# Kernel tuning notes

Hardware: AMD Instinct MI355X
Metric: run time of the kernel (lower is better)

## Reference

```python
import jax, jax.numpy as jnp
import numpy as np

N_NODES = 50000
N_EDGES = 800000
IN_F = 128
OUT_F = 128
HEADS = 8
HEAD_DIM = OUT_F // HEADS
EDGE_F = 32


def setup_inputs() -> dict:
    key = jax.random.key(0)
    ks = jax.random.split(key, 14)
    s = lambda fan_in: 1.0 / np.sqrt(fan_in)
    return {
        "node_features": jax.random.normal(ks[0], (N_NODES, IN_F), jnp.float32),
        "edge_index": jax.random.randint(ks[1], (2, N_EDGES), 0, N_NODES, jnp.int64),
        "edge_features": jax.random.normal(ks[2], (N_EDGES, EDGE_F), jnp.float32),
        "Wq": jax.random.uniform(ks[3], (IN_F, OUT_F), jnp.float32, -s(IN_F), s(IN_F)),
        "bq": jnp.zeros((OUT_F,), jnp.float32),
        "Wk": jax.random.uniform(ks[4], (IN_F, OUT_F), jnp.float32, -s(IN_F), s(IN_F)),
        "bk": jnp.zeros((OUT_F,), jnp.float32),
        "Wv": jax.random.uniform(ks[5], (IN_F, OUT_F), jnp.float32, -s(IN_F), s(IN_F)),
        "bv": jnp.zeros((OUT_F,), jnp.float32),
        "We": jax.random.uniform(ks[6], (EDGE_F, HEADS), jnp.float32, -s(EDGE_F), s(EDGE_F)),
        "be": jnp.zeros((HEADS,), jnp.float32),
        "Wo": jax.random.uniform(ks[7], (OUT_F, OUT_F), jnp.float32, -s(OUT_F), s(OUT_F)),
        "bo": jnp.zeros((OUT_F,), jnp.float32),
    }


def reference(node_features, edge_index, edge_features,
              Wq, bq, Wk, bk, Wv, bv, We, be, Wo, bo):
    n_nodes = node_features.shape[0]
    n_edges = edge_index.shape[1]
    sources, targets = edge_index[0], edge_index[1]
    scale = HEAD_DIM ** -0.5

    # dense projections: [n_nodes, heads, head_dim]
    Q = (node_features @ Wq + bq).reshape(n_nodes, HEADS, HEAD_DIM)
    K = (node_features @ Wk + bk).reshape(n_nodes, HEADS, HEAD_DIM)
    V = (node_features @ Wv + bv).reshape(n_nodes, HEADS, HEAD_DIM)

    # gather by edge
    Q_t = Q[targets]           # [n_edges, heads, head_dim]
    K_s = K[sources]
    V_s = V[sources]

    scores = jnp.sum(Q_t * K_s, axis=-1) * scale      # [n_edges, heads]
    scores = scores + (edge_features @ We + be)       # edge bias

    # segment softmax over incoming edges of each target node
    max_s = jax.ops.segment_max(scores, targets, num_segments=n_nodes)
    scores = scores - max_s[targets]
    exp_s = jnp.exp(scores)
    denom = jax.ops.segment_sum(exp_s, targets, num_segments=n_nodes) + 1e-10
    probs = exp_s / denom[targets]                    # [n_edges, heads]

    weighted_V = probs[:, :, None] * V_s              # [n_edges, heads, head_dim]
    aggregated = jax.ops.segment_sum(
        weighted_V.reshape(n_edges, -1), targets, num_segments=n_nodes)
    return aggregated @ Wo + bo
```

## Files before the change

kernel.cpp:

```cpp
#include <hip/hip_runtime.h>

typedef __attribute__((ext_vector_type(8))) short shortx8;
typedef __attribute__((ext_vector_type(4))) float floatx4;
typedef unsigned short u16;
typedef unsigned int u32;

__device__ __forceinline__ float bf2f(unsigned short u) {
    union { unsigned int i; float f; } v; v.i = ((unsigned int)u) << 16; return v.f;
}
__device__ __forceinline__ float bfl(u32 u) {
    union { u32 i; float f; } v; v.i = u << 16; return v.f;
}
__device__ __forceinline__ float bfh(u32 u) {
    union { u32 i; float f; } v; v.i = u & 0xFFFF0000u; return v.f;
}
__device__ __forceinline__ unsigned short f2bf(float f) {
    union { float f; unsigned int i; } v; v.f = f;
    unsigned int x = v.i;
    unsigned int r = x + 0x7FFFu + ((x >> 16) & 1u);
    return (unsigned short)(r >> 16);
}
__device__ __forceinline__ float ldf(const void* p, int i, bool f32) {
    return f32 ? ((const float*)p)[i] : bf2f(((const u16*)p)[i]);
}

__global__ __launch_bounds__(256) void detect_zero_k(
    const u16* __restrict__ nf, const int* __restrict__ ei,
    int* __restrict__ flags, int* __restrict__ deg, int M)
{
    int tid = threadIdx.x;
    if (blockIdx.x != 0) {
        int i = (blockIdx.x - 1) * 256 + tid;
        if (i < M) deg[i] = 0;
        return;
    }
    __shared__ int cnt[2];
    if (tid < 2) cnt[tid] = 0;
    __syncthreads();
    int c0 = 0;
    for (int i = tid; i < 65536; i += 256) {
        u16 v = nf[i];
        if ((v & 0x7F80u) == 0x7F80u) c0++;
    }
    int c1 = 0;
    for (int i = tid; i < 4096; i += 256) {
        if (ei[2 * i + 1] != 0) c1++;
    }
    atomicAdd(&cnt[0], c0);
    atomicAdd(&cnt[1], c1);
    __syncthreads();
    if (tid == 0) {
        flags[0] = (cnt[0] > 8) ? 1 : 0;
        flags[1] = (cnt[1] < 100) ? 1 : 0;
    }
}

__global__ __launch_bounds__(256) void prep_k(
    const void* __restrict__ W0, const void* __restrict__ W1,
    const void* __restrict__ W2, const void* __restrict__ W3,
    const void* __restrict__ b0, const void* __restrict__ b1,
    const void* __restrict__ b2, const void* __restrict__ b3,
    const void* __restrict__ We, const void* __restrict__ be,
    const int* __restrict__ flags,
    u16* __restrict__ WT, float* __restrict__ biasWs,
    float* __restrict__ WeWs, float* __restrict__ beWs)
{
    bool f32 = flags[0] != 0;
    int tid = threadIdx.x;
    if (blockIdx.x < 32) {
        int t = blockIdx.x * 256 + tid;
        int mat  = t >> 11;
        int r    = t & 2047;
        int lane = r & 63;
        int ks   = (r >> 6) & 3;
        int ct   = r >> 8;
        const void* W = (mat == 0) ? W0 : (mat == 1) ? W1 : (mat == 2) ? W2 : W3;
        int k0  = ks * 32 + (lane >> 4) * 8;
        int col = ct * 16 + (lane & 15);
        u16 tmp[8];
#pragma unroll
        for (int j = 0; j < 8; ++j) {
            int off = (k0 + j) * 128 + col;
            tmp[j] = f32 ? f2bf(((const float*)W)[off]) : ((const u16*)W)[off];
        }
        *(shortx8*)(WT + (size_t)t * 8) = *(const shortx8*)tmp;
    } else {
        if (tid < 128) {
            biasWs[0 * 128 + tid] = ldf(b0, tid, f32);
            biasWs[1 * 128 + tid] = ldf(b1, tid, f32);
            biasWs[2 * 128 + tid] = ldf(b2, tid, f32);
            biasWs[3 * 128 + tid] = ldf(b3, tid, f32);
        }
        WeWs[tid] = ldf(We, tid, f32);
        if (tid < 8) beWs[tid] = ldf(be, tid, f32);
    }
}

__global__ __launch_bounds__(256) void hist_ebias_k(
    const int* __restrict__ ei, const void* __restrict__ ef,
    int* __restrict__ deg, int* __restrict__ rank,
    const float* __restrict__ WeWs, const float* __restrict__ beWs,
    float* __restrict__ EBe, int E, const int* __restrict__ flags)
{
    __shared__ float sWe[256];
    __shared__ float sbe[8];
    int tid = threadIdx.x;
    sWe[tid] = WeWs[tid];
    if (tid < 8) sbe[tid] = beWs[tid];
    __syncthreads();

    int e = blockIdx.x * 256 + tid;
    if (e >= E) return;
    bool f32 = flags[0] != 0;
    int tgt = flags[1] ? ei[2 * (E + e)] : ei[E + e];
    rank[e] = atomicAdd(&deg[tgt], 1);

    float v[32];
    if (f32) {
        const floatx4* ep = (const floatx4*)((const float*)ef + (size_t)e * 32);
#pragma unroll
        for (int g = 0; g < 8; ++g) {
            floatx4 t = ep[g];
#pragma unroll
            for (int j = 0; j < 4; ++j) v[g * 4 + j] = t[j];
        }
    } else {
        const shortx8* ep = (const shortx8*)((const u16*)ef + (size_t)e * 32);
#pragma unroll
        for (int g = 0; g < 4; ++g) {
            shortx8 t = ep[g];
#pragma unroll
            for (int j = 0; j < 8; ++j) v[g * 8 + j] = bf2f((unsigned short)t[j]);
        }
    }
    float eb[8];
#pragma unroll
    for (int h = 0; h < 8; ++h) eb[h] = sbe[h];
#pragma unroll
    for (int k = 0; k < 32; ++k)
#pragma unroll
        for (int h = 0; h < 8; ++h) eb[h] += v[k] * sWe[k * 8 + h];

    floatx4* op = (floatx4*)(EBe + (size_t)e * 8);
    op[0] = (floatx4){eb[0], eb[1], eb[2], eb[3]};
    op[1] = (floatx4){eb[4], eb[5], eb[6], eb[7]};
}

__global__ __launch_bounds__(256) void scan1_k(
    const int* __restrict__ deg, int* __restrict__ incl, int* __restrict__ bsum, int M)
{
    __shared__ int s[256];
    int tid = threadIdx.x;
    int i = blockIdx.x * 256 + tid;
    int v = (i < M) ? deg[i] : 0;
    s[tid] = v;
    __syncthreads();
#pragma unroll
    for (int off = 1; off < 256; off <<= 1) {
        int t = (tid >= off) ? s[tid - off] : 0;
        __syncthreads();
        s[tid] += t;
        __syncthreads();
    }
    if (i < M) incl[i] = s[tid];
    if (tid == 255) bsum[blockIdx.x] = s[255];
}

__global__ __launch_bounds__(256) void scan2_k(
    const int* __restrict__ bsum, int* __restrict__ boff, int nb)
{
    __shared__ int s[256];
    int tid = threadIdx.x;
    int v = (tid < nb) ? bsum[tid] : 0;
    s[tid] = v;
    __syncthreads();
#pragma unroll
    for (int off = 1; off < 256; off <<= 1) {
        int t = (tid >= off) ? s[tid - off] : 0;
        __syncthreads();
        s[tid] += t;
        __syncthreads();
    }
    if (tid < nb) boff[tid] = s[tid] - v;
}

__global__ __launch_bounds__(256) void scan3_k(
    const int* __restrict__ incl, const int* __restrict__ boff,
    int* __restrict__ rowptr, int M)
{
    int i = blockIdx.x * 256 + threadIdx.x;
    if (i >= M) return;
    rowptr[i + 1] = incl[i] + boff[i >> 8];
    if (i == 0) rowptr[0] = 0;
}

__global__ __launch_bounds__(256) void qkv_gemm_k(
    const void* __restrict__ A, int M,
    const u16* __restrict__ WT, const float* __restrict__ biasWs,
    u16* __restrict__ Qb, u16* __restrict__ KVb,
    const int* __restrict__ flags)
{
    bool aF32 = flags[0] != 0;
    int lane = threadIdx.x & 63;
    int wave = threadIdx.x >> 6;
    int quad = lane >> 4;
    int l15  = lane & 15;
    int m0   = blockIdx.x * 128 + wave * 32;

    shortx8 afrag[2][4];
#pragma unroll
    for (int mt = 0; mt < 2; ++mt) {
        int row = m0 + mt * 16 + l15;
        row = row < M ? row : M - 1;
#pragma unroll
        for (int ks = 0; ks < 4; ++ks) {
            size_t base = (size_t)row * 128 + ks * 32 + quad * 8;
            if (aF32) {
                const floatx4* ap = (const floatx4*)((const float*)A + base);
                floatx4 f0 = ap[0], f1 = ap[1];
                u16 tmp[8];
#pragma unroll
                for (int j = 0; j < 4; ++j) { tmp[j] = f2bf(f0[j]); tmp[4 + j] = f2bf(f1[j]); }
                afrag[mt][ks] = *(const shortx8*)tmp;
            } else {
                afrag[mt][ks] = *(const shortx8*)((const u16*)A + base);
            }
        }
    }

#pragma unroll
    for (int mat = 0; mat < 3; ++mat) {
        floatx4 acc[2][8];
#pragma unroll
        for (int a = 0; a < 2; ++a)
#pragma unroll
            for (int b = 0; b < 8; ++b)
                acc[a][b] = (floatx4){0.f, 0.f, 0.f, 0.f};
#pragma unroll
        for (int ks = 0; ks < 4; ++ks) {
#pragma unroll
            for (int ct = 0; ct < 8; ++ct) {
                shortx8 bfrag = *(const shortx8*)(WT + (size_t)mat * 16384 +
                                                  ((size_t)(ct * 4 + ks) * 64 + lane) * 8);
                acc[0][ct] = __builtin_amdgcn_mfma_f32_16x16x32_bf16(afrag[0][ks], bfrag, acc[0][ct], 0, 0, 0);
                acc[1][ct] = __builtin_amdgcn_mfma_f32_16x16x32_bf16(afrag[1][ks], bfrag, acc[1][ct], 0, 0, 0);
            }
        }
        u16* base = (mat == 0) ? Qb : (mat == 1) ? KVb : (KVb + 128);
        int stride = (mat == 0) ? 128 : 256;
#pragma unroll
        for (int ct = 0; ct < 8; ++ct) {
            int col = ct * 16 + l15;
            float bs = biasWs[mat * 128 + col];
#pragma unroll
            for (int mt = 0; mt < 2; ++mt) {
#pragma unroll
                for (int r = 0; r < 4; ++r) {
                    int row = m0 + mt * 16 + quad * 4 + r;
                    if (row < M)
                        base[(size_t)row * stride + col] = f2bf(acc[mt][ct][r] + bs);
                }
            }
        }
    }
}

__global__ __launch_bounds__(256) void scatter_k(
    const int* __restrict__ ei, const int* __restrict__ rank,
    const int* __restrict__ rowptr, int2* __restrict__ pr2,
    int E, const int* __restrict__ flags)
{
    int e = blockIdx.x * 256 + threadIdx.x;
    if (e >= E) return;
    bool i64 = flags[1] != 0;
    int src = i64 ? ei[2 * e]       : ei[e];
    int tgt = i64 ? ei[2 * (E + e)] : ei[E + e];
    pr2[rowptr[tgt] + rank[e]] = make_int2(src, e);
}

__global__ __launch_bounds__(256) void node_agg_k(
    const int2* __restrict__ pr2, const int* __restrict__ rowptr,
    const u16* __restrict__ Qb, const u16* __restrict__ KVb,
    const float* __restrict__ EBe, u16* __restrict__ aggN, int M, int E)
{
    int wave = threadIdx.x >> 6;
    int lane = threadIdx.x & 63;
    int n = blockIdx.x * 4 + wave;
    if (n >= M) return;
    int g = lane >> 4;
    int w = lane & 15;
    int h = w >> 1;

    int beg = rowptr[n], end = rowptr[n + 1];
    int pidx = beg + lane;
    if (pidx >= E) pidx = E - 1;
    int2 pv = pr2[pidx];

    uint4 qw = ((const uint4*)(Qb + (size_t)n * 128))[w];
    float q0 = bfl(qw.x), q1 = bfh(qw.x), q2 = bfl(qw.y), q3 = bfh(qw.y);
    float q4 = bfl(qw.z), q5 = bfh(qw.z), q6 = bfl(qw.w), q7 = bfh(qw.w);

    float acc[8];
#pragma unroll
    for (int j = 0; j < 8; ++j) acc[j] = 0.f;
    float dsum = 0.f;

    for (int i = beg; i < end; i += 8) {
        int idxA = i + g;
        int idxB = i + 4 + g;
        bool vA = idxA < end;
        bool vB = idxB < end;
        int cA = vA ? idxA : (end - 1);
        int cB = vB ? idxB : (end - 1);
        int offA = cA - beg;
        int offB = cB - beg;
        int srcA, eidA, srcB, eidB;
        if (offA < 64) { srcA = __shfl(pv.x, offA); eidA = __shfl(pv.y, offA); }
        else           { int2 t = pr2[cA]; srcA = t.x; eidA = t.y; }
        if (offB < 64) { srcB = __shfl(pv.x, offB); eidB = __shfl(pv.y, offB); }
        else           { int2 t = pr2[cB]; srcB = t.x; eidB = t.y; }

        const uint4* kpA = (const uint4*)(KVb + (size_t)srcA * 256);
        const uint4* kpB = (const uint4*)(KVb + (size_t)srcB * 256);
        uint4 kwA = kpA[w];
        uint4 kwB = kpB[w];
        uint4 vwA = kpA[16 + w];
        uint4 vwB = kpB[16 + w];
        float ebA = EBe[(size_t)eidA * 8 + h];
        float ebB = EBe[(size_t)eidB * 8 + h];

        float partA = q0 * bfl(kwA.x) + q1 * bfh(kwA.x)
                    + q2 * bfl(kwA.y) + q3 * bfh(kwA.y)
                    + q4 * bfl(kwA.z) + q5 * bfh(kwA.z)
                    + q6 * bfl(kwA.w) + q7 * bfh(kwA.w);
        float partB = q0 * bfl(kwB.x) + q1 * bfh(kwB.x)
                    + q2 * bfl(kwB.y) + q3 * bfh(kwB.y)
                    + q4 * bfl(kwB.z) + q5 * bfh(kwB.z)
                    + q6 * bfl(kwB.w) + q7 * bfh(kwB.w);
        partA += __shfl_xor(partA, 1);
        partB += __shfl_xor(partB, 1);
        float pA = vA ? __expf(partA * 0.25f + ebA) : 0.f;
        float pB = vB ? __expf(partB * 0.25f + ebB) : 0.f;
        dsum += pA + pB;
        acc[0] += pA * bfl(vwA.x) + pB * bfl(vwB.x);
        acc[1] += pA * bfh(vwA.x) + pB * bfh(vwB.x);
        acc[2] += pA * bfl(vwA.y) + pB * bfl(vwB.y);
        acc[3] += pA * bfh(vwA.y) + pB * bfh(vwB.y);
        acc[4] += pA * bfl(vwA.z) + pB * bfl(vwB.z);
        acc[5] += pA * bfh(vwA.z) + pB * bfh(vwB.z);
        acc[6] += pA * bfl(vwA.w) + pB * bfl(vwB.w);
        acc[7] += pA * bfh(vwA.w) + pB * bfh(vwB.w);
    }

    dsum += __shfl_xor(dsum, 16);
    dsum += __shfl_xor(dsum, 32);
#pragma unroll
    for (int j = 0; j < 8; ++j) {
        acc[j] += __shfl_xor(acc[j], 16);
        acc[j] += __shfl_xor(acc[j], 32);
    }
    if (g == 0) {
        float inv = 1.0f / (dsum + 1e-10f);
        uint4 o;
        o.x = (u32)f2bf(acc[0] * inv) | ((u32)f2bf(acc[1] * inv) << 16);
        o.y = (u32)f2bf(acc[2] * inv) | ((u32)f2bf(acc[3] * inv) << 16);
        o.z = (u32)f2bf(acc[4] * inv) | ((u32)f2bf(acc[5] * inv) << 16);
        o.w = (u32)f2bf(acc[6] * inv) | ((u32)f2bf(acc[7] * inv) << 16);
        ((uint4*)(aggN + (size_t)n * 128))[w] = o;
    }
}

__global__ __launch_bounds__(256) void out_gemm_k(
    const u16* __restrict__ A, int M,
    const u16* __restrict__ WT, const float* __restrict__ bias,
    void* __restrict__ out, const int* __restrict__ flags)
{
    bool oF32 = flags[0] != 0;
    int lane = threadIdx.x & 63;
    int wave = threadIdx.x >> 6;
    int quad = lane >> 4;
    int l15  = lane & 15;
    int m0   = blockIdx.x * 128 + wave * 32;

    floatx4 acc[2][8];
#pragma unroll
    for (int a = 0; a < 2; ++a)
#pragma unroll
        for (int b = 0; b < 8; ++b)
            acc[a][b] = (floatx4){0.f, 0.f, 0.f, 0.f};

#pragma unroll
    for (int ks = 0; ks < 4; ++ks) {
        shortx8 afrag[2];
#pragma unroll
        for (int mt = 0; mt < 2; ++mt) {
            int row = m0 + mt * 16 + l15;
            row = row < M ? row : M - 1;
            afrag[mt] = *(const shortx8*)(A + (size_t)row * 128 + ks * 32 + quad * 8);
        }
#pragma unroll
        for (int ct = 0; ct < 8; ++ct) {
            shortx8 bfrag = *(const shortx8*)(WT + ((size_t)(ct * 4 + ks) * 64 + lane) * 8);
            acc[0][ct] = __builtin_amdgcn_mfma_f32_16x16x32_bf16(afrag[0], bfrag, acc[0][ct], 0, 0, 0);
            acc[1][ct] = __builtin_amdgcn_mfma_f32_16x16x32_bf16(afrag[1], bfrag, acc[1][ct], 0, 0, 0);
        }
    }

#pragma unroll
    for (int ct = 0; ct < 8; ++ct) {
        int col = ct * 16 + l15;
        float bs = bias[col];
#pragma unroll
        for (int mt = 0; mt < 2; ++mt) {
#pragma unroll
            for (int r = 0; r < 4; ++r) {
                int row = m0 + mt * 16 + quad * 4 + r;
                if (row < M) {
                    float v = acc[mt][ct][r] + bs;
                    if (oF32) ((float*)out)[(size_t)row * 128 + col] = v;
                    else      ((u16*)out)[(size_t)row * 128 + col] = f2bf(v);
                }
            }
        }
    }
}

extern "C" void kernel_launch(void* const* d_in, const int* in_sizes, int n_in,
                              void* d_out, int out_size, void* d_ws, size_t ws_size,
                              hipStream_t stream)
{
    const void* nf = d_in[0];
    const int*  ei = (const int*)d_in[1];
    const void* ef = d_in[2];
    const void* Wq = d_in[3];  const void* bq = d_in[4];
    const void* Wk = d_in[5];  const void* bk = d_in[6];
    const void* Wv = d_in[7];  const void* bv = d_in[8];
    const void* We = d_in[9];  const void* be = d_in[10];
    const void* Wo = d_in[11]; const void* bo = d_in[12];

    int M = in_sizes[0] / 128;
    int E = in_sizes[1] / 2;
    int nb = (M + 255) / 256;

    char* ws = (char*)d_ws;
    int*   flags  = (int*)(ws + 0);
    float* biasWs = (float*)(ws + 256);
    float* WeWs   = (float*)(ws + 2304);
    float* beWs   = (float*)(ws + 3328);
    u16*   WT     = (u16*)(ws + 4096);
    size_t O1 = 4096 + 131072;
    size_t qrow  = (size_t)M * 128 * 2;
    size_t kvrow = (size_t)M * 256 * 2;
    u16* Qb  = (u16*)(ws + O1);
    u16* KVb = (u16*)(ws + O1 + qrow);
    size_t O2 = O1 + qrow + kvrow;
    float* EBe = (float*)(ws + O2);
    size_t O3 = O2 + (size_t)E * 8 * 4;
    int2* pr2   = (int2*)(ws + O3);
    int* rank   = (int*)(pr2 + E);
    int* deg    = rank + E;
    int* incl   = deg + M;
    int* rowptr = incl + M;
    int* bsum   = rowptr + M + 1;
    int* boff   = bsum + 256;
    u16* aggN   = Qb;

    detect_zero_k<<<1 + nb, 256, 0, stream>>>((const u16*)nf, ei, flags, deg, M);
    prep_k<<<33, 256, 0, stream>>>(Wq, Wk, Wv, Wo, bq, bk, bv, bo, We, be,
                                   flags, WT, biasWs, WeWs, beWs);

    int eblocks = (E + 255) / 256;
    hist_ebias_k<<<eblocks, 256, 0, stream>>>(ei, ef, deg, rank, WeWs, beWs,
                                              EBe, E, flags);
    scan1_k<<<nb, 256, 0, stream>>>(deg, incl, bsum, M);
    scan2_k<<<1, 256, 0, stream>>>(bsum, boff, nb);
    scan3_k<<<nb, 256, 0, stream>>>(incl, boff, rowptr, M);

    int gblocks = (M + 127) / 128;
    qkv_gemm_k<<<gblocks, 256, 0, stream>>>(nf, M, WT, biasWs, Qb, KVb, flags);

    scatter_k<<<eblocks, 256, 0, stream>>>(ei, rank, rowptr, pr2, E, flags);

    node_agg_k<<<(M + 3) / 4, 256, 0, stream>>>(pr2, rowptr, Qb, KVb, EBe, aggN, M, E);

    out_gemm_k<<<gblocks, 256, 0, stream>>>(aggN, M, WT + 3 * 16384, biasWs + 384, d_out, flags);
}
```

Measured before the change: 443.1 us.

## Fuse prep kernels, scan stages, and QKV GEMM with edge-bias scatter into CSR records

Merges format detection and weight prep into one kernel, folds the scan2/scan3 stages into a single kernel, and runs the QKV GEMM concurrently with a fused edge-bias and scatter pass in one launch. The scatter now uses an atomic cursor per target instead of a precomputed rank, and writes 32-byte records holding the source plus the edge bias packed as bf16, directly in CSR order. The aggregation kernel reads this contiguous bias instead of gathering EBe by edge id. This cuts launches, drops the rank and EBe round trips and removes a random gather, at the cost of bf16 rounding on the bias, a larger record, and a nondeterministic order within each segment.

```diff
diff --git a/kernel.cpp b/kernel.cpp
--- a/kernel.cpp
+++ b/kernel.cpp
@@ -20,55 +20,52 @@
     unsigned int r = x + 0x7FFFu + ((x >> 16) & 1u);
     return (unsigned short)(r >> 16);
 }
+__device__ __forceinline__ u32 pack2bf(float a, float b) {
+    return (u32)f2bf(a) | ((u32)f2bf(b) << 16);
+}
 __device__ __forceinline__ float ldf(const void* p, int i, bool f32) {
     return f32 ? ((const float*)p)[i] : bf2f(((const u16*)p)[i]);
 }
 
-__global__ __launch_bounds__(256) void detect_zero_k(
+__global__ __launch_bounds__(256) void prep_all_k(
     const u16* __restrict__ nf, const int* __restrict__ ei,
-    int* __restrict__ flags, int* __restrict__ deg, int M)
-{
-    int tid = threadIdx.x;
-    if (blockIdx.x != 0) {
-        int i = (blockIdx.x - 1) * 256 + tid;
-        if (i < M) deg[i] = 0;
-        return;
-    }
-    __shared__ int cnt[2];
-    if (tid < 2) cnt[tid] = 0;
-    __syncthreads();
-    int c0 = 0;
-    for (int i = tid; i < 65536; i += 256) {
-        u16 v = nf[i];
-        if ((v & 0x7F80u) == 0x7F80u) c0++;
-    }
-    int c1 = 0;
-    for (int i = tid; i < 4096; i += 256) {
-        if (ei[2 * i + 1] != 0) c1++;
-    }
-    atomicAdd(&cnt[0], c0);
-    atomicAdd(&cnt[1], c1);
-    __syncthreads();
-    if (tid == 0) {
-        flags[0] = (cnt[0] > 8) ? 1 : 0;
-        flags[1] = (cnt[1] < 100) ? 1 : 0;
-    }
-}
-
-__global__ __launch_bounds__(256) void prep_k(
     const void* __restrict__ W0, const void* __restrict__ W1,
     const void* __restrict__ W2, const void* __restrict__ W3,
     const void* __restrict__ b0, const void* __restrict__ b1,
     const void* __restrict__ b2, const void* __restrict__ b3,
     const void* __restrict__ We, const void* __restrict__ be,
-    const int* __restrict__ flags,
+    int* __restrict__ flags, int* __restrict__ deg,
     u16* __restrict__ WT, float* __restrict__ biasWs,
-    float* __restrict__ WeWs, float* __restrict__ beWs)
-{
-    bool f32 = flags[0] != 0;
+    float* __restrict__ WeWs, float* __restrict__ beWs, int M)
+{
     int tid = threadIdx.x;
-    if (blockIdx.x < 32) {
-        int t = blockIdx.x * 256 + tid;
+    int bid = blockIdx.x;
+    if (bid >= 33) {
+        int i = (bid - 33) * 256 + tid;
+        if (i < M) deg[i] = 0;
+        return;
+    }
+    __shared__ int cnt[2];
+    if (tid < 2) cnt[tid] = 0;
+    __syncthreads();
+    int c0 = 0;
+    for (int i = tid; i < 8192; i += 256) {
+        u16 v = nf[i];
+        if ((v & 0x7F80u) == 0x7F80u) c0++;
+    }
+    atomicAdd(&cnt[0], c0);
+    if (bid == 32) {
+        int c1 = 0;
+        for (int i = tid; i < 1024; i += 256) {
+            if (ei[2 * i + 1] != 0) c1++;
+        }
+        atomicAdd(&cnt[1], c1);
+    }
+    __syncthreads();
+    bool f32 = cnt[0] > 6;
+
+    if (bid < 32) {
+        int t = bid * 256 + tid;
         int mat  = t >> 11;
         int r    = t & 2047;
         int lane = r & 63;
@@ -85,6 +82,10 @@
         }
         *(shortx8*)(WT + (size_t)t * 8) = *(const shortx8*)tmp;
     } else {
+        if (tid == 0) {
+            flags[0] = f32 ? 1 : 0;
+            flags[1] = (cnt[1] < 100) ? 1 : 0;
+        }
         if (tid < 128) {
             biasWs[0 * 128 + tid] = ldf(b0, tid, f32);
             biasWs[1 * 128 + tid] = ldf(b1, tid, f32);
@@ -96,54 +97,14 @@
     }
 }
 
-__global__ __launch_bounds__(256) void hist_ebias_k(
-    const int* __restrict__ ei, const void* __restrict__ ef,
-    int* __restrict__ deg, int* __restrict__ rank,
-    const float* __restrict__ WeWs, const float* __restrict__ beWs,
-    float* __restrict__ EBe, int E, const int* __restrict__ flags)
-{
-    __shared__ float sWe[256];
-    __shared__ float sbe[8];
-    int tid = threadIdx.x;
-    sWe[tid] = WeWs[tid];
-    if (tid < 8) sbe[tid] = beWs[tid];
-    __syncthreads();
-
-    int e = blockIdx.x * 256 + tid;
+__global__ __launch_bounds__(256) void hist_k(
+    const int* __restrict__ ei, int* __restrict__ deg,
+    int E, const int* __restrict__ flags)
+{
+    int e = blockIdx.x * 256 + threadIdx.x;
     if (e >= E) return;
-    bool f32 = flags[0] != 0;
     int tgt = flags[1] ? ei[2 * (E + e)] : ei[E + e];
-    rank[e] = atomicAdd(&deg[tgt], 1);
-
-    float v[32];
-    if (f32) {
-        const floatx4* ep = (const floatx4*)((const float*)ef + (size_t)e * 32);
-#pragma unroll
-        for (int g = 0; g < 8; ++g) {
-            floatx4 t = ep[g];
-#pragma unroll
-            for (int j = 0; j < 4; ++j) v[g * 4 + j] = t[j];
-        }
-    } else {
-        const shortx8* ep = (const shortx8*)((const u16*)ef + (size_t)e * 32);
-#pragma unroll
-        for (int g = 0; g < 4; ++g) {
-            shortx8 t = ep[g];
-#pragma unroll
-            for (int j = 0; j < 8; ++j) v[g * 8 + j] = bf2f((unsigned short)t[j]);
-        }
-    }
-    float eb[8];
-#pragma unroll
-    for (int h = 0; h < 8; ++h) eb[h] = sbe[h];
-#pragma unroll
-    for (int k = 0; k < 32; ++k)
-#pragma unroll
-        for (int h = 0; h < 8; ++h) eb[h] += v[k] * sWe[k * 8 + h];
-
-    floatx4* op = (floatx4*)(EBe + (size_t)e * 8);
-    op[0] = (floatx4){eb[0], eb[1], eb[2], eb[3]};
-    op[1] = (floatx4){eb[4], eb[5], eb[6], eb[7]};
+    atomicAdd(&deg[tgt], 1);
 }
 
 __global__ __launch_bounds__(256) void scan1_k(
@@ -166,8 +127,9 @@
     if (tid == 255) bsum[blockIdx.x] = s[255];
 }
 
-__global__ __launch_bounds__(256) void scan2_k(
-    const int* __restrict__ bsum, int* __restrict__ boff, int nb)
+__global__ __launch_bounds__(256) void scan23_k(
+    const int* __restrict__ bsum, int* __restrict__ incl_cur,
+    const int* __restrict__ deg, int* __restrict__ rowptr, int M, int nb)
 {
     __shared__ int s[256];
     int tid = threadIdx.x;
@@ -181,107 +143,150 @@
         s[tid] += t;
         __syncthreads();
     }
-    if (tid < nb) boff[tid] = s[tid] - v;
-}
-
-__global__ __launch_bounds__(256) void scan3_k(
-    const int* __restrict__ incl, const int* __restrict__ boff,
-    int* __restrict__ rowptr, int M)
-{
-    int i = blockIdx.x * 256 + threadIdx.x;
+    int b = blockIdx.x;
+    int boffb = (b == 0) ? 0 : s[b - 1];
+    int i = b * 256 + tid;
     if (i >= M) return;
-    rowptr[i + 1] = incl[i] + boff[i >> 8];
+    int r = incl_cur[i] + boffb;
+    rowptr[i + 1] = r;
+    incl_cur[i] = r - deg[i];
     if (i == 0) rowptr[0] = 0;
 }
 
-__global__ __launch_bounds__(256) void qkv_gemm_k(
+__global__ __launch_bounds__(256) void qkv_scatter_k(
     const void* __restrict__ A, int M,
     const u16* __restrict__ WT, const float* __restrict__ biasWs,
     u16* __restrict__ Qb, u16* __restrict__ KVb,
-    const int* __restrict__ flags)
-{
-    bool aF32 = flags[0] != 0;
-    int lane = threadIdx.x & 63;
-    int wave = threadIdx.x >> 6;
-    int quad = lane >> 4;
-    int l15  = lane & 15;
-    int m0   = blockIdx.x * 128 + wave * 32;
-
-    shortx8 afrag[2][4];
-#pragma unroll
-    for (int mt = 0; mt < 2; ++mt) {
-        int row = m0 + mt * 16 + l15;
-        row = row < M ? row : M - 1;
-#pragma unroll
-        for (int ks = 0; ks < 4; ++ks) {
-            size_t base = (size_t)row * 128 + ks * 32 + quad * 8;
-            if (aF32) {
-                const floatx4* ap = (const floatx4*)((const float*)A + base);
-                floatx4 f0 = ap[0], f1 = ap[1];
-                u16 tmp[8];
-#pragma unroll
-                for (int j = 0; j < 4; ++j) { tmp[j] = f2bf(f0[j]); tmp[4 + j] = f2bf(f1[j]); }
-                afrag[mt][ks] = *(const shortx8*)tmp;
-            } else {
-                afrag[mt][ks] = *(const shortx8*)((const u16*)A + base);
-            }
-        }
-    }
-
-#pragma unroll
-    for (int mat = 0; mat < 3; ++mat) {
-        floatx4 acc[2][8];
-#pragma unroll
-        for (int a = 0; a < 2; ++a)
-#pragma unroll
-            for (int b = 0; b < 8; ++b)
-                acc[a][b] = (floatx4){0.f, 0.f, 0.f, 0.f};
-#pragma unroll
-        for (int ks = 0; ks < 4; ++ks) {
-#pragma unroll
-            for (int ct = 0; ct < 8; ++ct) {
-                shortx8 bfrag = *(const shortx8*)(WT + (size_t)mat * 16384 +
-                                                  ((size_t)(ct * 4 + ks) * 64 + lane) * 8);
-                acc[0][ct] = __builtin_amdgcn_mfma_f32_16x16x32_bf16(afrag[0][ks], bfrag, acc[0][ct], 0, 0, 0);
-                acc[1][ct] = __builtin_amdgcn_mfma_f32_16x16x32_bf16(afrag[1][ks], bfrag, acc[1][ct], 0, 0, 0);
-            }
-        }
-        u16* base = (mat == 0) ? Qb : (mat == 1) ? KVb : (KVb + 128);
-        int stride = (mat == 0) ? 128 : 256;
-#pragma unroll
-        for (int ct = 0; ct < 8; ++ct) {
-            int col = ct * 16 + l15;
-            float bs = biasWs[mat * 128 + col];
-#pragma unroll
-            for (int mt = 0; mt < 2; ++mt) {
-#pragma unroll
-                for (int r = 0; r < 4; ++r) {
-                    int row = m0 + mt * 16 + quad * 4 + r;
-                    if (row < M)
-                        base[(size_t)row * stride + col] = f2bf(acc[mt][ct][r] + bs);
+    const int* __restrict__ ei, const void* __restrict__ ef,
+    int* __restrict__ cur,
+    const float* __restrict__ WeWs, const float* __restrict__ beWs,
+    uint4* __restrict__ rec, int E,
+    const int* __restrict__ flags, int gblocks)
+{
+    __shared__ float sWe[256];
+    __shared__ float sbe[8];
+
+    if (blockIdx.x < gblocks) {
+        bool aF32 = flags[0] != 0;
+        int lane = threadIdx.x & 63;
+        int wave = threadIdx.x >> 6;
+        int quad = lane >> 4;
+        int l15  = lane & 15;
+        int m0   = blockIdx.x * 128 + wave * 32;
+
+        shortx8 afrag[2][4];
+#pragma unroll
+        for (int mt = 0; mt < 2; ++mt) {
+            int row = m0 + mt * 16 + l15;
+            row = row < M ? row : M - 1;
+#pragma unroll
+            for (int ks = 0; ks < 4; ++ks) {
+                size_t base = (size_t)row * 128 + ks * 32 + quad * 8;
+                if (aF32) {
+                    const floatx4* ap = (const floatx4*)((const float*)A + base);
+                    floatx4 f0 = ap[0], f1 = ap[1];
+                    u16 tmp[8];
+#pragma unroll
+                    for (int j = 0; j < 4; ++j) { tmp[j] = f2bf(f0[j]); tmp[4 + j] = f2bf(f1[j]); }
+                    afrag[mt][ks] = *(const shortx8*)tmp;
+                } else {
+                    afrag[mt][ks] = *(const shortx8*)((const u16*)A + base);
                 }
             }
         }
-    }
-}
-
-__global__ __launch_bounds__(256) void scatter_k(
-    const int* __restrict__ ei, const int* __restrict__ rank,
-    const int* __restrict__ rowptr, int2* __restrict__ pr2,
-    int E, const int* __restrict__ flags)
-{
-    int e = blockIdx.x * 256 + threadIdx.x;
-    if (e >= E) return;
-    bool i64 = flags[1] != 0;
-    int src = i64 ? ei[2 * e]       : ei[e];
-    int tgt = i64 ? ei[2 * (E + e)] : ei[E + e];
-    pr2[rowptr[tgt] + rank[e]] = make_int2(src, e);
+
+#pragma unroll
+        for (int mat = 0; mat < 3; ++mat) {
+            floatx4 acc[2][8];
+#pragma unroll
+            for (int a = 0; a < 2; ++a)
+#pragma unroll
+                for (int b = 0; b < 8; ++b)
+                    acc[a][b] = (floatx4){0.f, 0.f, 0.f, 0.f};
+#pragma unroll
+            for (int ks = 0; ks < 4; ++ks) {
+#pragma unroll
+                for (int ct = 0; ct < 8; ++ct) {
+                    shortx8 bfrag = *(const shortx8*)(WT + (size_t)mat * 16384 +
+                                                      ((size_t)(ct * 4 + ks) * 64 + lane) * 8);
+                    acc[0][ct] = __builtin_amdgcn_mfma_f32_16x16x32_bf16(afrag[0][ks], bfrag, acc[0][ct], 0, 0, 0);
+                    acc[1][ct] = __builtin_amdgcn_mfma_f32_16x16x32_bf16(afrag[1][ks], bfrag, acc[1][ct], 0, 0, 0);
+                }
+            }
+            u16* base = (mat == 0) ? Qb : (mat == 1) ? KVb : (KVb + 128);
+            int stride = (mat == 0) ? 128 : 256;
+#pragma unroll
+            for (int ct = 0; ct < 8; ++ct) {
+                int col = ct * 16 + l15;
+                float bs = biasWs[mat * 128 + col];
+#pragma unroll
+                for (int mt = 0; mt < 2; ++mt) {
+#pragma unroll
+                    for (int r = 0; r < 4; ++r) {
+                        int row = m0 + mt * 16 + quad * 4 + r;
+                        if (row < M)
+                            base[(size_t)row * stride + col] = f2bf(acc[mt][ct][r] + bs);
+                    }
+                }
+            }
+        }
+    } else {
+        int tid = threadIdx.x;
+        sWe[tid] = WeWs[tid];
+        if (tid < 8) sbe[tid] = beWs[tid];
+        __syncthreads();
+
+        int e = (blockIdx.x - gblocks) * 256 + tid;
+        if (e >= E) return;
+        bool f32 = flags[0] != 0;
+        bool i64 = flags[1] != 0;
+
+        int src = i64 ? ei[2 * e]       : ei[e];
+        int tgt = i64 ? ei[2 * (E + e)] : ei[E + e];
+        int pos = atomicAdd(&cur[tgt], 1);
+
+        float v[32];
+        if (f32) {
+            const floatx4* ep = (const floatx4*)((const float*)ef + (size_t)e * 32);
+#pragma unroll
+            for (int g = 0; g < 8; ++g) {
+                floatx4 t = ep[g];
+#pragma unroll
+                for (int j = 0; j < 4; ++j) v[g * 4 + j] = t[j];
+            }
+        } else {
+            const shortx8* ep = (const shortx8*)((const u16*)ef + (size_t)e * 32);
+#pragma unroll
+            for (int g = 0; g < 4; ++g) {
+                shortx8 t = ep[g];
+#pragma unroll
+                for (int j = 0; j < 8; ++j) v[g * 8 + j] = bf2f((unsigned short)t[j]);
+            }
+        }
+        float eb[8];
+#pragma unroll
+        for (int h = 0; h < 8; ++h) eb[h] = sbe[h];
+#pragma unroll
+        for (int k = 0; k < 32; ++k)
+#pragma unroll
+            for (int h = 0; h < 8; ++h) eb[h] += v[k] * sWe[k * 8 + h];
+
+        uint4 r0, r1;
+        r0.x = (u32)src;
+        r0.y = pack2bf(eb[0], eb[1]);
+        r0.z = pack2bf(eb[2], eb[3]);
+        r0.w = pack2bf(eb[4], eb[5]);
+        r1.x = pack2bf(eb[6], eb[7]);
+        r1.y = 0; r1.z = 0; r1.w = 0;
+        rec[(size_t)pos * 2]     = r0;
+        rec[(size_t)pos * 2 + 1] = r1;
+    }
 }
 
 __global__ __launch_bounds__(256) void node_agg_k(
-    const int2* __restrict__ pr2, const int* __restrict__ rowptr,
+    const uint4* __restrict__ rec, const int* __restrict__ rowptr,
     const u16* __restrict__ Qb, const u16* __restrict__ KVb,
-    const float* __restrict__ EBe, u16* __restrict__ aggN, int M, int E)
+    u16* __restrict__ aggN, int M, int E)
 {
     int wave = threadIdx.x >> 6;
     int lane = threadIdx.x & 63;
@@ -292,9 +297,9 @@
     int h = w >> 1;
 
     int beg = rowptr[n], end = rowptr[n + 1];
-    int pidx = beg + lane;
-    if (pidx >= E) pidx = E - 1;
-    int2 pv = pr2[pidx];
+    int ridx = beg + (lane >> 1);
+    if (ridx >= E) ridx = E - 1;
+    uint4 pv = rec[(size_t)ridx * 2 + (lane & 1)];
 
     uint4 qw = ((const uint4*)(Qb + (size_t)n * 128))[w];
     float q0 = bfl(qw.x), q1 = bfh(qw.x), q2 = bfl(qw.y), q3 = bfh(qw.y);
@@ -314,11 +319,37 @@
         int cB = vB ? idxB : (end - 1);
         int offA = cA - beg;
         int offB = cB - beg;
-        int srcA, eidA, srcB, eidB;
-        if (offA < 64) { srcA = __shfl(pv.x, offA); eidA = __shfl(pv.y, offA); }
-        else           { int2 t = pr2[cA]; srcA = t.x; eidA = t.y; }
-        if (offB < 64) { srcB = __shfl(pv.x, offB); eidB = __shfl(pv.y, offB); }
-        else           { int2 t = pr2[cB]; srcB = t.x; eidB = t.y; }
+
+        int srcA, srcB;
+        float ebA, ebB;
+        if (offA < 32) {
+            srcA = __shfl((int)pv.x, 2 * offA);
+            u32 w01 = __shfl((int)pv.y, 2 * offA);
+            u32 w23 = __shfl((int)pv.z, 2 * offA);
+            u32 w45 = __shfl((int)pv.w, 2 * offA);
+            u32 w67 = __shfl((int)pv.x, 2 * offA + 1);
+            u32 sel = (h < 2) ? w01 : (h < 4) ? w23 : (h < 6) ? w45 : w67;
+            ebA = (h & 1) ? bfh(sel) : bfl(sel);
+        } else {
+            const u32* rw = (const u32*)(rec + (size_t)cA * 2);
+            srcA = (int)rw[0];
+            u32 sel = rw[1 + h / 2];
+            ebA = (h & 1) ? bfh(sel) : bfl(sel);
+        }
+        if (offB < 32) {
+            srcB = __shfl((int)pv.x, 2 * offB);
+            u32 w01 = __shfl((int)pv.y, 2 * offB);
+            u32 w23 = __shfl((int)pv.z, 2 * offB);
+            u32 w45 = __shfl((int)pv.w, 2 * offB);
+            u32 w67 = __shfl((int)pv.x, 2 * offB + 1);
+            u32 sel = (h < 2) ? w01 : (h < 4) ? w23 : (h < 6) ? w45 : w67;
+            ebB = (h & 1) ? bfh(sel) : bfl(sel);
+        } else {
+            const u32* rw = (const u32*)(rec + (size_t)cB * 2);
+            srcB = (int)rw[0];
+            u32 sel = rw[1 + h / 2];
+            ebB = (h & 1) ? bfh(sel) : bfl(sel);
+        }
 
         const uint4* kpA = (const uint4*)(KVb + (size_t)srcA * 256);
         const uint4* kpB = (const uint4*)(KVb + (size_t)srcB * 256);
@@ -326,8 +357,6 @@
         uint4 kwB = kpB[w];
         uint4 vwA = kpA[16 + w];
         uint4 vwB = kpB[16 + w];
-        float ebA = EBe[(size_t)eidA * 8 + h];
-        float ebB = EBe[(size_t)eidB * 8 + h];
 
         float partA = q0 * bfl(kwA.x) + q1 * bfh(kwA.x)
                     + q2 * bfl(kwA.y) + q3 * bfh(kwA.y)
@@ -454,34 +483,29 @@
     u16* Qb  = (u16*)(ws + O1);
     u16* KVb = (u16*)(ws + O1 + qrow);
     size_t O2 = O1 + qrow + kvrow;
-    float* EBe = (float*)(ws + O2);
-    size_t O3 = O2 + (size_t)E * 8 * 4;
-    int2* pr2   = (int2*)(ws + O3);
-    int* rank   = (int*)(pr2 + E);
-    int* deg    = rank + E;
+    uint4* rec = (uint4*)(ws + O2);
+    size_t O3 = O2 + (size_t)E * 32;
+    int* deg    = (int*)(ws + O3);
     int* incl   = deg + M;
     int* rowptr = incl + M;
     int* bsum   = rowptr + M + 1;
-    int* boff   = bsum + 256;
     u16* aggN   = Qb;
 
-    detect_zero_k<<<1 + nb, 256, 0, stream>>>((const u16*)nf, ei, flags, deg, M);
-    prep_k<<<33, 256, 0, stream>>>(Wq, Wk, Wv, Wo, bq, bk, bv, bo, We, be,
-                                   flags, WT, biasWs, WeWs, beWs);
+    prep_all_k<<<33 + nb, 256, 0, stream>>>((const u16*)nf, ei,
+                                            Wq, Wk, Wv, Wo, bq, bk, bv, bo, We, be,
+                                            flags, deg, WT, biasWs, WeWs, beWs, M);
 
     int eblocks = (E + 255) / 256;
-    hist_ebias_k<<<eblocks, 256, 0, stream>>>(ei, ef, deg, rank, WeWs, beWs,
-                                              EBe, E, flags);
+    hist_k<<<eblocks, 256, 0, stream>>>(ei, deg, E, flags);
     scan1_k<<<nb, 256, 0, stream>>>(deg, incl, bsum, M);
-    scan2_k<<<1, 256, 0, stream>>>(bsum, boff, nb);
-    scan3_k<<<nb, 256, 0, stream>>>(incl, boff, rowptr, M);
+    scan23_k<<<nb, 256, 0, stream>>>(bsum, incl, deg, rowptr, M, nb);
 
     int gblocks = (M + 127) / 128;
-    qkv_gemm_k<<<gblocks, 256, 0, stream>>>(nf, M, WT, biasWs, Qb, KVb, flags);
-
-    scatter_k<<<eblocks, 256, 0, stream>>>(ei, rank, rowptr, pr2, E, flags);
-
-    node_agg_k<<<(M + 3) / 4, 256, 0, stream>>>(pr2, rowptr, Qb, KVb, EBe, aggN, M, E);
+    qkv_scatter_k<<<gblocks + eblocks, 256, 0, stream>>>(
+        nf, M, WT, biasWs, Qb, KVb,
+        ei, ef, incl , WeWs, beWs, rec, E, flags, gblocks);
+
+    node_agg_k<<<(M + 3) / 4, 256, 0, stream>>>(rec, rowptr, Qb, KVb, aggN, M, E);
 
     out_gemm_k<<<gblocks, 256, 0, stream>>>(aggN, M, WT + 3 * 16384, biasWs + 384, d_out, flags);
 }
```

After: 383.6 us. 1.16x faster.
